# Performance work log

Hardware: AMD Instinct MI355X
Metric: run time of the kernel (lower is better)

## Reference

```python
import jax, jax.numpy as jnp
import numpy as np

B, N, D_IN, D_OUT, H = 4, 2048, 1024, 1024, 16
HD = D_OUT // H

def _xavier(key, shape):
    fan_in, fan_out = shape[0], shape[1]
    a = jnp.sqrt(6.0 / (fan_in + fan_out))
    return jax.random.uniform(key, shape, jnp.float32, -a, a)

def setup_inputs() -> dict:
    key = jax.random.key(0)
    ks = jax.random.split(key, 6)
    x = jax.random.normal(ks[0], (B, N, D_IN), jnp.float32)
    w_q = _xavier(ks[1], (D_IN, D_OUT))
    w_k = _xavier(ks[2], (D_IN, D_OUT))
    w_v = _xavier(ks[3], (D_IN, D_OUT))
    # nn.Linear default init: uniform(-1/sqrt(fan_in), 1/sqrt(fan_in))
    bound = 1.0 / jnp.sqrt(D_OUT)
    w_o = jax.random.uniform(ks[4], (D_OUT, D_OUT), jnp.float32, -bound, bound)
    b_o = jax.random.uniform(ks[5], (D_OUT,), jnp.float32, -bound, bound)
    return {"x": x, "w_q": w_q, "w_k": w_k, "w_v": w_v, "w_o": w_o, "b_o": b_o}

def reference(x, w_q, w_k, w_v, w_o, b_o):
    b, n, _ = x.shape
    def split_heads(t):  # [b,n,D_OUT] -> [b,H,n,HD]
        return t.reshape(b, n, H, HD).transpose(0, 2, 1, 3)
    q = split_heads(x @ w_q)
    k = split_heads(x @ w_k)
    v = split_heads(x @ w_v)
    scores = jnp.einsum('bhqd,bhkd->bhqk', q, k) / jnp.sqrt(jnp.float32(HD))
    attn = jax.nn.softmax(scores, axis=-1)
    out = jnp.einsum('bhqk,bhkd->bhqd', attn, v)
    out = out.transpose(0, 2, 1, 3).reshape(b, n, D_OUT)
    return out @ w_o + b_o
```

## Files before the change

### kernel.cpp

```cpp
#include <hip/hip_runtime.h>
#include <stdint.h>
#include <stddef.h>

typedef __attribute__((ext_vector_type(8))) short bf16x8_t;
typedef __attribute__((ext_vector_type(4))) float f32x4_t;
typedef __attribute__((ext_vector_type(16))) float f32x16_t;
typedef __attribute__((ext_vector_type(4))) unsigned int u32x4_t;
typedef __attribute__((ext_vector_type(2))) unsigned int u32x2_t;

__device__ __forceinline__ unsigned short f2bf(float f) {
  union { float f; unsigned int u; } x; x.f = f;
  unsigned int r = x.u + 0x7fffu + ((x.u >> 16) & 1u);
  return (unsigned short)(r >> 16);
}

__device__ __forceinline__ float e2(float x) { return __builtin_amdgcn_exp2f(x); }

__device__ __forceinline__ unsigned int cvtpk(float lo, float hi) {
  unsigned int d;
  asm("v_cvt_pk_bf16_f32 %0, %1, %2" : "=v"(d) : "v"(lo), "v"(hi));
  return d;
}
__device__ __forceinline__ void plswap(unsigned int& a, unsigned int& b) {
  asm("v_permlane32_swap_b32 %0, %1" : "+v"(a), "+v"(b));
}

__device__ __forceinline__ void gload16(const void* g, void* l) {
  __builtin_amdgcn_global_load_lds(
      (const __attribute__((address_space(1))) void*)g,
      (__attribute__((address_space(3))) void*)l, 16, 0, 0);
}

#define QSCALE 0.18033688011112042f

__global__ __launch_bounds__(256)
void f32_to_bf16(const float* __restrict__ in, unsigned short* __restrict__ out) {
  size_t i = ((size_t)blockIdx.x * 256 + threadIdx.x) * 8;
  f32x4_t a = *(const f32x4_t*)(in + i);
  f32x4_t b = *(const f32x4_t*)(in + i + 4);
  bf16x8_t o;
#pragma unroll
  for (int j = 0; j < 4; ++j) { o[j] = (short)f2bf(a[j]); o[j + 4] = (short)f2bf(b[j]); }
  *(bf16x8_t*)(out + i) = o;
}

__global__ __launch_bounds__(256)
void transpose_cvt3(const float* __restrict__ w0, const float* __restrict__ w1,
                    const float* __restrict__ w2, unsigned short* __restrict__ out) {
  __shared__ float t[32][33];
  const float* in = blockIdx.z == 0 ? w0 : (blockIdx.z == 1 ? w1 : w2);
  unsigned short* o = out + (size_t)blockIdx.z * 1024 * 1024;
  const int x = threadIdx.x & 31, y = threadIdx.x >> 5;
  const int bx = blockIdx.x * 32, by = blockIdx.y * 32;
#pragma unroll
  for (int i = 0; i < 32; i += 8)
    t[y + i][x] = in[(size_t)(by + y + i) * 1024 + bx + x];
  __syncthreads();
#pragma unroll
  for (int i = 0; i < 32; i += 8)
    o[(size_t)(bx + y + i) * 1024 + by + x] = f2bf(t[x][y + i]);
}

__global__ __launch_bounds__(256)
void transpose_cvt(const float* __restrict__ in, unsigned short* __restrict__ out) {
  __shared__ float t[32][33];
  const int x = threadIdx.x & 31, y = threadIdx.x >> 5;
  const int bx = blockIdx.x * 32, by = blockIdx.y * 32;
#pragma unroll
  for (int i = 0; i < 32; i += 8)
    t[y + i][x] = in[(size_t)(by + y + i) * 1024 + bx + x];
  __syncthreads();
#pragma unroll
  for (int i = 0; i < 32; i += 8)
    out[(size_t)(bx + y + i) * 1024 + by + x] = f2bf(t[x][y + i]);
}

__global__ __launch_bounds__(256)
void transpose_v(const unsigned short* __restrict__ in, unsigned short* __restrict__ out) {
  __shared__ unsigned short t[64][65];
  const int bh = blockIdx.y;
  const int n0 = blockIdx.x * 64;
  const int c = threadIdx.x & 63, r4 = threadIdx.x >> 6;
#pragma unroll
  for (int i = 0; i < 64; i += 4)
    t[r4 + i][c] = in[((size_t)bh * 2048 + n0 + r4 + i) * 64 + c];
  __syncthreads();
#pragma unroll
  for (int i = 0; i < 64; i += 4)
    out[((size_t)bh * 64 + r4 + i) * 2048 + n0 + c] = t[c][r4 + i];
}

template <int MODE>
__global__ __launch_bounds__(512, 4)
void gemm256(const unsigned short* __restrict__ A,
             const unsigned short* __restrict__ Bt,
             void* __restrict__ Cv,
             const float* __restrict__ bias,
             int M, int K, int Nn, int rowTiles) {
  __shared__ __align__(16) unsigned short As[2][256 * 32];
  __shared__ __align__(16) unsigned short Bs[2][128 * 32];

  const int tid = threadIdx.x;
  const int wave = tid >> 6;
  const int lane = tid & 63;
  const int l15 = lane & 15;
  const int lq = lane >> 4;

  const int bid = blockIdx.x;
  const int xcd = bid & 7, tb = bid >> 3;
  const int row0 = (xcd * rowTiles + (tb % rowTiles)) * 256;
  const int col0 = (tb / rowTiles) * 128;

  const int wr = (wave >> 1) * 64;
  const int wc = (wave & 1) * 64;

  f32x4_t acc[4][4];
#pragma unroll
  for (int m = 0; m < 4; ++m)
#pragma unroll
    for (int n = 0; n < 4; ++n) acc[m][n] = (f32x4_t)0.f;

  const int pa0 = tid, pa1 = tid + 512, pb = tid;
  const int ra0 = pa0 >> 2, sa0 = (pa0 & 3) ^ (ra0 & 3);
  const int ra1 = pa1 >> 2, sa1 = (pa1 & 3) ^ (ra1 & 3);
  const int rb  = pb >> 2,  sb  = (pb & 3) ^ (rb & 3);

  const unsigned short* Ap0 = A + (size_t)(row0 + ra0) * K + sa0 * 8;
  const unsigned short* Ap1 = A + (size_t)(row0 + ra1) * K + sa1 * 8;
  const unsigned short* Bp0 = Bt + (size_t)(col0 + rb) * K + sb * 8;

  gload16(Ap0, (char*)As[0] + pa0 * 16);
  gload16(Ap1, (char*)As[0] + pa1 * 16);
  gload16(Bp0, (char*)Bs[0] + pb * 16);
  __syncthreads();

  const int NIT = K / 32;
  for (int it = 0; it < NIT; ++it) {
    const int cur = it & 1;
    if (it + 1 < NIT) {
      const int k0n = (it + 1) * 32;
      gload16(Ap0 + k0n, (char*)As[cur ^ 1] + pa0 * 16);
      gload16(Ap1 + k0n, (char*)As[cur ^ 1] + pa1 * 16);
      gload16(Bp0 + k0n, (char*)Bs[cur ^ 1] + pb * 16);
    }

    const char* Ac = (const char*)As[cur];
    const char* Bc = (const char*)Bs[cur];
    bf16x8_t af[4], bfr[4];
#pragma unroll
    for (int m = 0; m < 4; ++m) {
      int r = wr + m * 16 + l15;
      af[m] = *(const bf16x8_t*)(Ac + r * 64 + ((lq ^ (r & 3)) << 4));
    }
#pragma unroll
    for (int n = 0; n < 4; ++n) {
      int c = wc + n * 16 + l15;
      bfr[n] = *(const bf16x8_t*)(Bc + c * 64 + ((lq ^ (c & 3)) << 4));
    }
    __builtin_amdgcn_s_setprio(1);
#pragma unroll
    for (int m = 0; m < 4; ++m)
#pragma unroll
      for (int n = 0; n < 4; ++n)
        acc[m][n] = __builtin_amdgcn_mfma_f32_16x16x32_bf16(af[m], bfr[n], acc[m][n], 0, 0, 0);
    __builtin_amdgcn_s_setprio(0);

    __syncthreads();
  }

#pragma unroll
  for (int m = 0; m < 4; ++m) {
    int rbase = row0 + wr + m * 16 + lq * 4;
#pragma unroll
    for (int n = 0; n < 4; ++n) {
      int col = col0 + wc + n * 16 + l15;
#pragma unroll
      for (int j = 0; j < 4; ++j) {
        int row = rbase + j;
        float v = acc[m][n][j];
        if constexpr (MODE == 0) {
          int which = col >> 10, cl = col & 1023;
          int b = row >> 11, nn = row & 2047, h = cl >> 6, hd = cl & 63;
          float s = (which == 0) ? QSCALE : 1.0f;
          ((unsigned short*)Cv)[(size_t)which * 8388608 +
                                (((size_t)(b * 16 + h)) * 2048 + nn) * 64 + hd] = f2bf(v * s);
        } else {
          ((float*)Cv)[(size_t)row * Nn + col] = v + bias[col];
        }
      }
    }
  }
}

__global__ __launch_bounds__(512, 4)
void attn_mfma(const unsigned short* __restrict__ qb,
               const unsigned short* __restrict__ kb,
               const unsigned short* __restrict__ vtb,
               unsigned short* __restrict__ ab) {
  __shared__ __align__(16) unsigned short Ks[2][8192];
  __shared__ __align__(16) unsigned short Vs[2][8192];

  const int tid = threadIdx.x, wave = tid >> 6, lane = tid & 63;
  const int l31 = lane & 31, hi = lane >> 5;

  const int bid = blockIdx.x;
  const int xcd = bid & 7, w = bid >> 3;
  const int bh = xcd * 8 + (w >> 3);
  const int q0 = (w & 7) * 256;

  const unsigned short* qrow = qb + ((size_t)bh * 2048 + q0 + wave * 32 + l31) * 64;
  bf16x8_t qf[4];
#pragma unroll
  for (int ks = 0; ks < 4; ++ks)
    qf[ks] = *(const bf16x8_t*)(qrow + ks * 16 + hi * 8);

  f32x16_t O[2];
#pragma unroll
  for (int hb = 0; hb < 2; ++hb) O[hb] = (f32x16_t)0.f;
  float m_run = -1e30f, l_run = 0.f;

  const unsigned short* kbase = kb + (size_t)bh * 2048 * 64;
  const unsigned short* vbase = vtb + (size_t)bh * 64 * 2048;
  int koff[2], voff[2];
#pragma unroll
  for (int i = 0; i < 2; ++i) {
    int c = tid + 512 * i;
    int kr = c >> 3, kp = c & 7, kl = kp ^ (kr & 7);
    koff[i] = kr * 64 + kl * 8;
    int vr = c >> 4, vp = c & 15, vl = (vp & 8) | ((vp & 7) ^ (vr & 7));
    voff[i] = vr * 2048 + vl * 8;
  }

#pragma unroll
  for (int i = 0; i < 2; ++i) {
    gload16(kbase + koff[i], (char*)Ks[0] + (tid + 512 * i) * 16);
    gload16(vbase + voff[i], (char*)Vs[0] + (tid + 512 * i) * 16);
  }
  __syncthreads();

  for (int t = 0; t < 16; ++t) {
    const int cur = t & 1;
    if (t < 15) {
      const unsigned short* kt = kbase + (size_t)(t + 1) * 8192;
      const unsigned short* vt = vbase + (t + 1) * 128;
#pragma unroll
      for (int i = 0; i < 2; ++i) {
        gload16(kt + koff[i], (char*)Ks[cur ^ 1] + (tid + 512 * i) * 16);
        gload16(vt + voff[i], (char*)Vs[cur ^ 1] + (tid + 512 * i) * 16);
      }
    }
    const char* Kc = (const char*)Ks[cur];
    const char* Vc = (const char*)Vs[cur];

    f32x16_t sacc[4];
#pragma unroll
    for (int kbk = 0; kbk < 4; ++kbk) sacc[kbk] = (f32x16_t)0.f;
    __builtin_amdgcn_s_setprio(1);
#pragma unroll
    for (int kbk = 0; kbk < 4; ++kbk) {
#pragma unroll
      for (int ks = 0; ks < 4; ++ks) {
        int key = kbk * 32 + l31;
        bf16x8_t kf = *(const bf16x8_t*)(Kc + key * 128 + (((ks * 2 + hi) ^ (key & 7)) << 4));
        sacc[kbk] = __builtin_amdgcn_mfma_f32_32x32x16_bf16(kf, qf[ks], sacc[kbk], 0, 0, 0);
      }
    }
    __builtin_amdgcn_s_setprio(0);

    float mk[4];
#pragma unroll
    for (int kbk = 0; kbk < 4; ++kbk) {
      float a0 = fmaxf(sacc[kbk][0], sacc[kbk][8]);
      float a1 = fmaxf(sacc[kbk][1], sacc[kbk][9]);
      float a2 = fmaxf(sacc[kbk][2], sacc[kbk][10]);
      float a3 = fmaxf(sacc[kbk][3], sacc[kbk][11]);
      float a4 = fmaxf(sacc[kbk][4], sacc[kbk][12]);
      float a5 = fmaxf(sacc[kbk][5], sacc[kbk][13]);
      float a6 = fmaxf(sacc[kbk][6], sacc[kbk][14]);
      float a7 = fmaxf(sacc[kbk][7], sacc[kbk][15]);
      a0 = fmaxf(a0, a4); a1 = fmaxf(a1, a5); a2 = fmaxf(a2, a6); a3 = fmaxf(a3, a7);
      mk[kbk] = fmaxf(fmaxf(a0, a1), fmaxf(a2, a3));
    }
    float mx = fmaxf(fmaxf(mk[0], mk[1]), fmaxf(mk[2], mk[3]));
    mx = fmaxf(mx, __shfl_xor(mx, 32));

    const float mn = fmaxf(m_run, mx);
    const float alpha = e2(m_run - mn);
    m_run = mn;
    l_run *= alpha;
#pragma unroll
    for (int hb = 0; hb < 2; ++hb)
#pragma unroll
      for (int r = 0; r < 16; ++r) O[hb][r] *= alpha;

    float psum = 0.f;
#pragma unroll
    for (int kbk = 0; kbk < 4; ++kbk) {
      float p[16];
#pragma unroll
      for (int r = 0; r < 16; ++r) p[r] = e2(sacc[kbk][r] - mn);
      float s0 = p[0] + p[8],  s1 = p[1] + p[9],  s2 = p[2] + p[10], s3 = p[3] + p[11];
      float s4 = p[4] + p[12], s5 = p[5] + p[13], s6 = p[6] + p[14], s7 = p[7] + p[15];
      s0 += s4; s1 += s5; s2 += s6; s3 += s7;
      psum += (s0 + s1) + (s2 + s3);
#pragma unroll
      for (int u = 0; u < 2; ++u) {
        unsigned int a0 = cvtpk(p[8 * u + 0], p[8 * u + 1]);
        unsigned int b0 = cvtpk(p[8 * u + 4], p[8 * u + 5]);
        plswap(a0, b0);
        unsigned int a1 = cvtpk(p[8 * u + 2], p[8 * u + 3]);
        unsigned int b1 = cvtpk(p[8 * u + 6], p[8 * u + 7]);
        plswap(a1, b1);
        u32x4_t fw; fw[0] = a0; fw[1] = a1; fw[2] = b0; fw[3] = b1;
        bf16x8_t pfrag = *(bf16x8_t*)&fw;
        const int ks2 = kbk * 2 + u;
        __builtin_amdgcn_s_setprio(1);
#pragma unroll
        for (int hb = 0; hb < 2; ++hb) {
          int hd = hb * 32 + l31;
          int sl = ks2 * 2 + hi;
          bf16x8_t vf = *(const bf16x8_t*)(Vc + hd * 256 +
                          (((sl & 8) | ((sl & 7) ^ (hd & 7))) << 4));
          O[hb] = __builtin_amdgcn_mfma_f32_32x32x16_bf16(vf, pfrag, O[hb], 0, 0, 0);
        }
        __builtin_amdgcn_s_setprio(0);
      }
    }
    psum += __shfl_xor(psum, 32);
    l_run += psum;

    __syncthreads();
  }

  const int b = bh >> 4, h = bh & 15;
  const float inv = 1.f / l_run;
  const int row = q0 + wave * 32 + l31;
  unsigned short* op = ab + ((size_t)(b * 2048 + row)) * 1024 + h * 64;
#pragma unroll
  for (int hb = 0; hb < 2; ++hb)
#pragma unroll
    for (int tt = 0; tt < 4; ++tt) {
      u32x2_t d;
      d[0] = cvtpk(O[hb][4 * tt + 0] * inv, O[hb][4 * tt + 1] * inv);
      d[1] = cvtpk(O[hb][4 * tt + 2] * inv, O[hb][4 * tt + 3] * inv);
      *(u32x2_t*)(op + hb * 32 + tt * 8 + hi * 4) = d;
    }
}

extern "C" void kernel_launch(void* const* d_in, const int* in_sizes, int n_in,
                              void* d_out, int out_size, void* d_ws, size_t ws_size,
                              hipStream_t stream) {
  const float* x  = (const float*)d_in[0];
  const float* wq = (const float*)d_in[1];
  const float* wk = (const float*)d_in[2];
  const float* wv = (const float*)d_in[3];
  const float* wo = (const float*)d_in[4];
  const float* bo = (const float*)d_in[5];
  float* out = (float*)d_out;

  const size_t MB = 1ull << 20;
  char* ws = (char*)d_ws;
  unsigned short* xb  = (unsigned short*)(ws);
  unsigned short* ab  = xb;
  unsigned short* qkv = (unsigned short*)(ws + 17 * MB);
  unsigned short* vtb = (unsigned short*)(ws + 68 * MB);
  unsigned short* wT  = (unsigned short*)(ws + 85 * MB);
  unsigned short* woT = (unsigned short*)(ws + 91 * MB);

  const size_t X = 8388608;

  const dim3 tb(256);
  f32_to_bf16<<<4096, tb, 0, stream>>>(x, xb);
  transpose_cvt3<<<dim3(32, 32, 3), tb, 0, stream>>>(wq, wk, wv, wT);
  transpose_cvt<<<dim3(32, 32), tb, 0, stream>>>(wo, woT);

  gemm256<0><<<dim3(768), dim3(512), 0, stream>>>(xb, wT, (void*)qkv, nullptr,
                                                  8192, 1024, 3072, 4);

  transpose_v<<<dim3(32, 64), tb, 0, stream>>>(qkv + 2 * X, vtb);

  attn_mfma<<<dim3(512), dim3(512), 0, stream>>>(qkv, qkv + X, vtb, ab);

  gemm256<1><<<dim3(256), dim3(512), 0, stream>>>(ab, woT, (void*)out, bo,
                                                  8192, 1024, 1024, 4);
}
```

Measured before the change: 309.5 us.

## Deepen GEMM K-tile to 64 with dynamic LDS, merge weight transposes, drop setprio

The GEMM now stages a K=64 slice per iteration in 96 KB of dynamic shared memory with an 8-way XOR swizzle. This halves the number of barrier-separated iterations and doubles the MFMA work done between syncs. The launch bound drops to one block per CU, so latency hiding relies on fewer waves. Separately, the Wo transpose is folded into a single four-way transpose launch, and the s_setprio hints are removed from the attention kernel.

```diff
diff --git a/kernel.cpp b/kernel.cpp
--- a/kernel.cpp
+++ b/kernel.cpp
@@ -45,11 +45,13 @@
 }
 
 __global__ __launch_bounds__(256)
-void transpose_cvt3(const float* __restrict__ w0, const float* __restrict__ w1,
-                    const float* __restrict__ w2, unsigned short* __restrict__ out) {
+void transpose_cvt4(const float* __restrict__ w0, const float* __restrict__ w1,
+                    const float* __restrict__ w2, const float* __restrict__ w3,
+                    unsigned short* __restrict__ wT, unsigned short* __restrict__ woT) {
   __shared__ float t[32][33];
-  const float* in = blockIdx.z == 0 ? w0 : (blockIdx.z == 1 ? w1 : w2);
-  unsigned short* o = out + (size_t)blockIdx.z * 1024 * 1024;
+  const int z = blockIdx.z;
+  const float* in = (z == 0) ? w0 : (z == 1) ? w1 : (z == 2) ? w2 : w3;
+  unsigned short* o = (z < 3) ? (wT + (size_t)z * 1024 * 1024) : woT;
   const int x = threadIdx.x & 31, y = threadIdx.x >> 5;
   const int bx = blockIdx.x * 32, by = blockIdx.y * 32;
 #pragma unroll
@@ -59,20 +61,6 @@
 #pragma unroll
   for (int i = 0; i < 32; i += 8)
     o[(size_t)(bx + y + i) * 1024 + by + x] = f2bf(t[x][y + i]);
-}
-
-__global__ __launch_bounds__(256)
-void transpose_cvt(const float* __restrict__ in, unsigned short* __restrict__ out) {
-  __shared__ float t[32][33];
-  const int x = threadIdx.x & 31, y = threadIdx.x >> 5;
-  const int bx = blockIdx.x * 32, by = blockIdx.y * 32;
-#pragma unroll
-  for (int i = 0; i < 32; i += 8)
-    t[y + i][x] = in[(size_t)(by + y + i) * 1024 + bx + x];
-  __syncthreads();
-#pragma unroll
-  for (int i = 0; i < 32; i += 8)
-    out[(size_t)(bx + y + i) * 1024 + by + x] = f2bf(t[x][y + i]);
 }
 
 __global__ __launch_bounds__(256)
@@ -91,14 +79,17 @@
 }
 
 template <int MODE>
-__global__ __launch_bounds__(512, 4)
+__global__ __launch_bounds__(512, 1)
 void gemm256(const unsigned short* __restrict__ A,
              const unsigned short* __restrict__ Bt,
              void* __restrict__ Cv,
              const float* __restrict__ bias,
              int M, int K, int Nn, int rowTiles) {
-  __shared__ __align__(16) unsigned short As[2][256 * 32];
-  __shared__ __align__(16) unsigned short Bs[2][128 * 32];
+  extern __shared__ __align__(16) char smem[];
+  char* Abuf0 = smem;
+  char* Abuf1 = smem + 32768;
+  char* Bbuf0 = smem + 65536;
+  char* Bbuf1 = smem + 81920;
 
   const int tid = threadIdx.x;
   const int wave = tid >> 6;
@@ -120,50 +111,61 @@
 #pragma unroll
     for (int n = 0; n < 4; ++n) acc[m][n] = (f32x4_t)0.f;
 
-  const int pa0 = tid, pa1 = tid + 512, pb = tid;
-  const int ra0 = pa0 >> 2, sa0 = (pa0 & 3) ^ (ra0 & 3);
-  const int ra1 = pa1 >> 2, sa1 = (pa1 & 3) ^ (ra1 & 3);
-  const int rb  = pb >> 2,  sb  = (pb & 3) ^ (rb & 3);
-
-  const unsigned short* Ap0 = A + (size_t)(row0 + ra0) * K + sa0 * 8;
-  const unsigned short* Ap1 = A + (size_t)(row0 + ra1) * K + sa1 * 8;
-  const unsigned short* Bp0 = Bt + (size_t)(col0 + rb) * K + sb * 8;
-
-  gload16(Ap0, (char*)As[0] + pa0 * 16);
-  gload16(Ap1, (char*)As[0] + pa1 * 16);
-  gload16(Bp0, (char*)Bs[0] + pb * 16);
+  const unsigned short* Apt[4];
+  const unsigned short* Bpt[2];
+#pragma unroll
+  for (int i = 0; i < 4; ++i) {
+    int c = tid + 512 * i;
+    int r = c >> 3, s = (c & 7) ^ (r & 7);
+    Apt[i] = A + (size_t)(row0 + r) * K + s * 8;
+  }
+#pragma unroll
+  for (int i = 0; i < 2; ++i) {
+    int c = tid + 512 * i;
+    int r = c >> 3, s = (c & 7) ^ (r & 7);
+    Bpt[i] = Bt + (size_t)(col0 + r) * K + s * 8;
+  }
+
+#pragma unroll
+  for (int i = 0; i < 4; ++i) gload16(Apt[i], Abuf0 + (tid + 512 * i) * 16);
+#pragma unroll
+  for (int i = 0; i < 2; ++i) gload16(Bpt[i], Bbuf0 + (tid + 512 * i) * 16);
   __syncthreads();
 
-  const int NIT = K / 32;
+  const int NIT = K >> 6;
   for (int it = 0; it < NIT; ++it) {
     const int cur = it & 1;
+    char* Ac = cur ? Abuf1 : Abuf0;
+    char* Bc = cur ? Bbuf1 : Bbuf0;
     if (it + 1 < NIT) {
-      const int k0n = (it + 1) * 32;
-      gload16(Ap0 + k0n, (char*)As[cur ^ 1] + pa0 * 16);
-      gload16(Ap1 + k0n, (char*)As[cur ^ 1] + pa1 * 16);
-      gload16(Bp0 + k0n, (char*)Bs[cur ^ 1] + pb * 16);
-    }
-
-    const char* Ac = (const char*)As[cur];
-    const char* Bc = (const char*)Bs[cur];
-    bf16x8_t af[4], bfr[4];
-#pragma unroll
-    for (int m = 0; m < 4; ++m) {
-      int r = wr + m * 16 + l15;
-      af[m] = *(const bf16x8_t*)(Ac + r * 64 + ((lq ^ (r & 3)) << 4));
-    }
-#pragma unroll
-    for (int n = 0; n < 4; ++n) {
-      int c = wc + n * 16 + l15;
-      bfr[n] = *(const bf16x8_t*)(Bc + c * 64 + ((lq ^ (c & 3)) << 4));
-    }
-    __builtin_amdgcn_s_setprio(1);
-#pragma unroll
-    for (int m = 0; m < 4; ++m)
-#pragma unroll
-      for (int n = 0; n < 4; ++n)
-        acc[m][n] = __builtin_amdgcn_mfma_f32_16x16x32_bf16(af[m], bfr[n], acc[m][n], 0, 0, 0);
-    __builtin_amdgcn_s_setprio(0);
+      const int k0n = (it + 1) * 64;
+      char* An = cur ? Abuf0 : Abuf1;
+      char* Bn = cur ? Bbuf0 : Bbuf1;
+#pragma unroll
+      for (int i = 0; i < 4; ++i) gload16(Apt[i] + k0n, An + (tid + 512 * i) * 16);
+#pragma unroll
+      for (int i = 0; i < 2; ++i) gload16(Bpt[i] + k0n, Bn + (tid + 512 * i) * 16);
+    }
+
+#pragma unroll
+    for (int ks2 = 0; ks2 < 2; ++ks2) {
+      bf16x8_t af[4], bfr[4];
+#pragma unroll
+      for (int m = 0; m < 4; ++m) {
+        int r = wr + m * 16 + l15;
+        af[m] = *(const bf16x8_t*)(Ac + r * 128 + (((ks2 * 4 + lq) ^ (r & 7)) << 4));
+      }
+#pragma unroll
+      for (int n = 0; n < 4; ++n) {
+        int c = wc + n * 16 + l15;
+        bfr[n] = *(const bf16x8_t*)(Bc + c * 128 + (((ks2 * 4 + lq) ^ (c & 7)) << 4));
+      }
+#pragma unroll
+      for (int m = 0; m < 4; ++m)
+#pragma unroll
+        for (int n = 0; n < 4; ++n)
+          acc[m][n] = __builtin_amdgcn_mfma_f32_16x16x32_bf16(af[m], bfr[n], acc[m][n], 0, 0, 0);
+    }
 
     __syncthreads();
   }
@@ -255,7 +257,6 @@
     f32x16_t sacc[4];
 #pragma unroll
     for (int kbk = 0; kbk < 4; ++kbk) sacc[kbk] = (f32x16_t)0.f;
-    __builtin_amdgcn_s_setprio(1);
 #pragma unroll
     for (int kbk = 0; kbk < 4; ++kbk) {
 #pragma unroll
@@ -265,7 +266,6 @@
         sacc[kbk] = __builtin_amdgcn_mfma_f32_32x32x16_bf16(kf, qf[ks], sacc[kbk], 0, 0, 0);
       }
     }
-    __builtin_amdgcn_s_setprio(0);
 
     float mk[4];
 #pragma unroll
@@ -314,7 +314,6 @@
         u32x4_t fw; fw[0] = a0; fw[1] = a1; fw[2] = b0; fw[3] = b1;
         bf16x8_t pfrag = *(bf16x8_t*)&fw;
         const int ks2 = kbk * 2 + u;
-        __builtin_amdgcn_s_setprio(1);
 #pragma unroll
         for (int hb = 0; hb < 2; ++hb) {
           int hd = hb * 32 + l31;
@@ -323,7 +322,6 @@
                           (((sl & 8) | ((sl & 7) ^ (hd & 7))) << 4));
           O[hb] = __builtin_amdgcn_mfma_f32_32x32x16_bf16(vf, pfrag, O[hb], 0, 0, 0);
         }
-        __builtin_amdgcn_s_setprio(0);
       }
     }
     psum += __shfl_xor(psum, 32);
@@ -371,16 +369,15 @@
 
   const dim3 tb(256);
   f32_to_bf16<<<4096, tb, 0, stream>>>(x, xb);
-  transpose_cvt3<<<dim3(32, 32, 3), tb, 0, stream>>>(wq, wk, wv, wT);
-  transpose_cvt<<<dim3(32, 32), tb, 0, stream>>>(wo, woT);
-
-  gemm256<0><<<dim3(768), dim3(512), 0, stream>>>(xb, wT, (void*)qkv, nullptr,
-                                                  8192, 1024, 3072, 4);
+  transpose_cvt4<<<dim3(32, 32, 4), tb, 0, stream>>>(wq, wk, wv, wo, wT, woT);
+
+  gemm256<0><<<dim3(768), dim3(512), 98304, stream>>>(xb, wT, (void*)qkv, nullptr,
+                                                      8192, 1024, 3072, 4);
 
   transpose_v<<<dim3(32, 64), tb, 0, stream>>>(qkv + 2 * X, vtb);
 
   attn_mfma<<<dim3(512), dim3(512), 0, stream>>>(qkv, qkv + X, vtb, ab);
 
-  gemm256<1><<<dim3(256), dim3(512), 0, stream>>>(ab, woT, (void*)out, bo,
-                                                  8192, 1024, 1024, 4);
-}
+  gemm256<1><<<dim3(256), dim3(512), 98304, stream>>>(ab, woT, (void*)out, bo,
+                                                      8192, 1024, 1024, 4);
+}
```

Result: faster. 287.1 us (-7.2%).
